# Performance work log

Measured on AMD Instinct MI355X. Metric: run time of the kernel, lower is better.

The kernel has to match this reference:

```python
import jax, jax.numpy as jnp
import numpy as np

N, D = 2048, 1024
H, KV, HD = 16, 4, 64
REPEATS = H // KV
SCALE = HD ** -0.5


def setup_inputs() -> dict:
    key = jax.random.key(0)
    ks = jax.random.split(key, 6)
    x = jax.random.normal(ks[0], (N, D), dtype=jnp.float32)
    # rotary tables: cos/sin of interleaved-pair angles (llama-style view_as_complex)
    pos = jnp.arange(N, dtype=jnp.float32)[:, None]
    inv_freq = 1.0 / (10000.0 ** (jnp.arange(0, HD, 2, dtype=jnp.float32) / HD))
    ang = pos * inv_freq[None, :]  # (N, HD//2)
    freqs_cos = jnp.cos(ang)
    freqs_sin = jnp.sin(ang)
    s = 0.02
    Wq = jax.random.normal(ks[1], (D, H * HD), dtype=jnp.float32) * s
    Wk = jax.random.normal(ks[2], (D, KV * HD), dtype=jnp.float32) * s
    Wv = jax.random.normal(ks[3], (D, KV * HD), dtype=jnp.float32) * s
    Wo = jax.random.normal(ks[4], (H * HD, D), dtype=jnp.float32) * s
    return {"x": x, "freqs_cos": freqs_cos, "freqs_sin": freqs_sin,
            "Wq": Wq, "Wk": Wk, "Wv": Wv, "Wo": Wo}


def _rope(t, cos, sin):
    # t: (N, heads, HD); interleaved complex pairs (even=real, odd=imag)
    tr = t[..., 0::2]
    ti = t[..., 1::2]
    c = cos[:, None, :]
    s = sin[:, None, :]
    out_r = tr * c - ti * s
    out_i = tr * s + ti * c
    return jnp.stack([out_r, out_i], axis=-1).reshape(t.shape)


def reference(x, freqs_cos, freqs_sin, Wq, Wk, Wv, Wo):
    n = x.shape[0]
    xq = (x @ Wq).reshape(n, H, HD)
    xk = (x @ Wk).reshape(n, KV, HD)
    xv = (x @ Wv).reshape(n, KV, HD)
    xq = _rope(xq, freqs_cos, freqs_sin)
    xk = _rope(xk, freqs_cos, freqs_sin)
    # repeat_kv along head dim (GQA)
    k = jnp.repeat(xk, REPEATS, axis=1)  # (n, H, HD)
    v = jnp.repeat(xv, REPEATS, axis=1)
    # memory_efficient_attention with mask=None: full attention over token axis
    scores = jnp.einsum('nhd,mhd->hnm', xq, k) * SCALE
    attn = jax.nn.softmax(scores, axis=-1)
    out = jnp.einsum('hnm,mhd->nhd', attn, v)
    return out.reshape(n, H * HD) @ Wo
```

## Files before the change

kernel.cpp:

```cpp
#include <hip/hip_runtime.h>

#define N_TOK 2048
#define DMODEL 1024
#define NH 16
#define NKV 4
#define HDIM 64
#define SCALE_LOG2E 0.1803368801111204f

typedef __attribute__((ext_vector_type(8))) short short8;
typedef __attribute__((ext_vector_type(4))) float f32x4;
typedef __attribute__((ext_vector_type(16))) float f32x16;
typedef __attribute__((ext_vector_type(2))) int i32x2;
typedef __attribute__((ext_vector_type(4))) unsigned int u32x4;
typedef unsigned short u16;
typedef unsigned int u32;

__device__ __forceinline__ u16 f2bf(float x) {
    u32 u = __float_as_uint(x);
    u += 0x7FFF + ((u >> 16) & 1);
    return (u16)(u >> 16);
}
__device__ __forceinline__ u32 pack2(float a, float b) {
    return (u32)f2bf(a) | ((u32)f2bf(b) << 16);
}
__device__ __forceinline__ u32 pack2t(float a, float b) {
    return __builtin_amdgcn_perm(__float_as_uint(b), __float_as_uint(a), 0x07060302u);
}

__device__ __forceinline__ void gload16(const u16* g, u16* l) {
    __builtin_amdgcn_global_load_lds(
        (const __attribute__((address_space(1))) unsigned int*)g,
        (__attribute__((address_space(3))) unsigned int*)l, 16, 0, 0);
}

__global__ __launch_bounds__(256) void prep(
    const float* __restrict__ Wq, const float* __restrict__ Wk,
    const float* __restrict__ Wv, const float* __restrict__ Wo,
    const float* __restrict__ x,
    u16* __restrict__ Wqt, u16* __restrict__ Wkt, u16* __restrict__ Wvt,
    u16* __restrict__ Wot, u16* __restrict__ xb)
{
    const int z = blockIdx.z;
    const int t = threadIdx.x;
    if (z == 4) {
        size_t base = ((size_t)(blockIdx.y * 16 + blockIdx.x)) * 8192;
#pragma unroll
        for (int i = 0; i < 8; ++i) {
            float4 v = *(const float4*)(x + base + i * 1024 + t * 4);
            uint2 p; p.x = pack2(v.x, v.y); p.y = pack2(v.z, v.w);
            *(uint2*)(xb + base + i * 1024 + t * 4) = p;
        }
        return;
    }
    const float* W; u16* Wt; int NC;
    if      (z == 0) { W = Wq; Wt = Wqt; NC = 1024; }
    else if (z == 1) { W = Wk; Wt = Wkt; NC = 256; }
    else if (z == 2) { W = Wv; Wt = Wvt; NC = 256; }
    else             { W = Wo; Wt = Wot; NC = 1024; }
    const int n0 = blockIdx.x * 64;
    if (n0 >= NC) return;
    const int k0 = blockIdx.y * 64;
    __shared__ float T[64][68];
    const int row = t >> 2, cs = (t & 3) * 16;
#pragma unroll
    for (int i = 0; i < 4; ++i)
        *(float4*)&T[row][cs + i * 4] =
            *(const float4*)(W + (size_t)(k0 + row) * NC + n0 + cs + i * 4);
    __syncthreads();
    const int nl = t >> 2, ks = (t & 3) * 16;
    u32 pk[8];
#pragma unroll
    for (int i = 0; i < 8; ++i)
        pk[i] = pack2(T[ks + 2 * i][nl], T[ks + 2 * i + 1][nl]);
    u16* dst = Wt + (size_t)(n0 + nl) * DMODEL + k0 + ks;
    uint4 w0; w0.x = pk[0]; w0.y = pk[1]; w0.z = pk[2]; w0.w = pk[3];
    uint4 w1; w1.x = pk[4]; w1.y = pk[5]; w1.z = pk[6]; w1.w = pk[7];
    *(uint4*)(dst) = w0;
    *(uint4*)(dst + 8) = w1;
}

__global__ __launch_bounds__(256, 3) void gemm_qkv(
    const u16* __restrict__ A,
    const u16* __restrict__ B0, const u16* __restrict__ B1, const u16* __restrict__ B2,
    u16* __restrict__ D0, u16* __restrict__ D1, u16* __restrict__ FVout,
    const float* __restrict__ fc, const float* __restrict__ fs)
{
    __shared__ u16 As[3][64][64];
    __shared__ u16 Bs[3][64][64];
    const int t = threadIdx.x;
    const int m0 = blockIdx.x * 64;
    const int by = blockIdx.y;

    const u16* Bt; int nl0, ep;
    u16* dbf = nullptr; int dstride = 0; float epsc = 1.f;
    if (by < 16)      { Bt = B0; nl0 = by * 64;        dbf = D0; ep = 1; dstride = 1024;
                        epsc = SCALE_LOG2E; }
    else if (by < 20) { Bt = B1; nl0 = (by - 16) * 64; dbf = D1; ep = 1; dstride = 256; }
    else              { Bt = B2; nl0 = (by - 20) * 64; ep = 2; }

    const int w = t >> 6, lane = t & 63;
    const int quad = lane >> 4, l15 = lane & 15;
    const int wm = (w >> 1) * 32, wn = (w & 1) * 32;
    const int rx = l15 & 7;

    const int sro = w * 16 + (lane >> 3);
    const int sco = ((lane & 7) ^ (lane >> 3)) * 8;
    const u16* ApL = A + (size_t)(m0 + sro) * DMODEL + sco;
    const u16* BpL = Bt + (size_t)(nl0 + sro) * DMODEL + sco;

    f32x4 acc[2][2];
#pragma unroll
    for (int i = 0; i < 2; ++i)
#pragma unroll
        for (int j = 0; j < 2; ++j) acc[i][j] = {0.f, 0.f, 0.f, 0.f};

#pragma unroll
    for (int k = 0; k < 2; ++k) {
        gload16(ApL + k * 8 * DMODEL, &As[0][w * 16 + k * 8][0]);
        gload16(BpL + k * 8 * DMODEL, &Bs[0][w * 16 + k * 8][0]);
    }
#pragma unroll
    for (int k = 0; k < 2; ++k) {
        gload16(ApL + k * 8 * DMODEL + 64, &As[1][w * 16 + k * 8][0]);
        gload16(BpL + k * 8 * DMODEL + 64, &Bs[1][w * 16 + k * 8][0]);
    }
    asm volatile("s_waitcnt vmcnt(4)" ::: "memory");
    __builtin_amdgcn_sched_barrier(0);
    __builtin_amdgcn_s_barrier();

    int cb = 0, nb = 1, pb = 2;
    for (int it = 0; it < 16; ++it) {
        if (it + 2 < 16) {
            const int kk = (it + 2) * 64;
#pragma unroll
            for (int k = 0; k < 2; ++k) {
                gload16(ApL + k * 8 * DMODEL + kk, &As[pb][w * 16 + k * 8][0]);
                gload16(BpL + k * 8 * DMODEL + kk, &Bs[pb][w * 16 + k * 8][0]);
            }
        }
#pragma unroll
        for (int c = 0; c < 2; ++c) {
            short8 af[2], bf[2];
#pragma unroll
            for (int i = 0; i < 2; ++i)
                af[i] = *(const short8*)&As[cb][wm + i * 16 + l15][((4 * c + quad) ^ rx) * 8];
#pragma unroll
            for (int j = 0; j < 2; ++j)
                bf[j] = *(const short8*)&Bs[cb][wn + j * 16 + l15][((4 * c + quad) ^ rx) * 8];
#pragma unroll
            for (int i = 0; i < 2; ++i)
#pragma unroll
                for (int j = 0; j < 2; ++j)
                    acc[i][j] = __builtin_amdgcn_mfma_f32_16x16x32_bf16(af[i], bf[j], acc[i][j], 0, 0, 0);
        }
        if (it + 2 < 16) asm volatile("s_waitcnt vmcnt(4)" ::: "memory");
        else             asm volatile("s_waitcnt vmcnt(0)" ::: "memory");
        __builtin_amdgcn_sched_barrier(0);
        __builtin_amdgcn_s_barrier();
        const int tmp = cb; cb = nb; nb = pb; pb = tmp;
    }

#pragma unroll
    for (int i = 0; i < 2; ++i)
#pragma unroll
        for (int j = 0; j < 2; ++j) {
            const int cl = nl0 + wn + j * 16 + l15;
            if (ep == 1) {
#pragma unroll
                for (int r4 = 0; r4 < 4; ++r4) {
                    const int r = m0 + wm + i * 16 + quad * 4 + r4;
                    float own = acc[i][j][r4];
                    float other = __shfl_xor(own, 1, 64);
                    const int p = (cl & 63) >> 1;
                    const float c = fc[r * 32 + p] * epsc, s = fs[r * 32 + p] * epsc;
                    float outv = ((cl & 1) == 0) ? (own * c - other * s)
                                                 : (other * s + own * c);
                    dbf[(size_t)r * dstride + cl] = f2bf(outv);
                }
            } else {
                const int rb = m0 + wm + i * 16 + quad * 4;
                const int g = cl >> 6, d = cl & 63;
                const int d2 = d >> 5, dl = d & 31;
                const int keyblk = rb >> 7, kg = (rb >> 5) & 3;
                const int kst = (rb >> 4) & 1, hb = (rb >> 3) & 1, jv = rb & 7;
                size_t idx = ((((((size_t)(g * 16 + keyblk) * 4 + kg) * 2 + kst) * 2 + d2)
                               * 2 + hb) * 32 + dl) * 8 + jv;
                uint2 pk;
                pk.x = pack2(acc[i][j][0], acc[i][j][1]);
                pk.y = pack2(acc[i][j][2], acc[i][j][3]);
                *(uint2*)(FVout + idx) = pk;
            }
        }
}

__global__ __launch_bounds__(256, 2) void gemm_out(
    const u16* __restrict__ A, const u16* __restrict__ Bt, float* __restrict__ Dout)
{
    __shared__ u16 As[3][64][64];
    __shared__ u16 Bs[3][64][64];
    const int t = threadIdx.x;
    const int m0 = blockIdx.x * 64;
    const int nl0 = blockIdx.y * 64;

    const int w = t >> 6, lane = t & 63;
    const int quad = lane >> 4, l15 = lane & 15;
    const int wm = (w >> 1) * 32, wn = (w & 1) * 32;
    const int rx = l15 & 7;

    const int sro = w * 16 + (lane >> 3);
    const int sco = ((lane & 7) ^ (lane >> 3)) * 8;
    const u16* ApL = A + (size_t)(m0 + sro) * DMODEL + sco;
    const u16* BpL = Bt + (size_t)(nl0 + sro) * DMODEL + sco;

    f32x4 acc[2][2];
#pragma unroll
    for (int i = 0; i < 2; ++i)
#pragma unroll
        for (int j = 0; j < 2; ++j) acc[i][j] = {0.f, 0.f, 0.f, 0.f};

#pragma unroll
    for (int k = 0; k < 2; ++k) {
        gload16(ApL + k * 8 * DMODEL, &As[0][w * 16 + k * 8][0]);
        gload16(BpL + k * 8 * DMODEL, &Bs[0][w * 16 + k * 8][0]);
    }
#pragma unroll
    for (int k = 0; k < 2; ++k) {
        gload16(ApL + k * 8 * DMODEL + 64, &As[1][w * 16 + k * 8][0]);
        gload16(BpL + k * 8 * DMODEL + 64, &Bs[1][w * 16 + k * 8][0]);
    }
    asm volatile("s_waitcnt vmcnt(4)" ::: "memory");
    __builtin_amdgcn_sched_barrier(0);
    __builtin_amdgcn_s_barrier();

    int cb = 0, nb = 1, pb = 2;
    for (int it = 0; it < 16; ++it) {
        if (it + 2 < 16) {
            const int kk = (it + 2) * 64;
#pragma unroll
            for (int k = 0; k < 2; ++k) {
                gload16(ApL + k * 8 * DMODEL + kk, &As[pb][w * 16 + k * 8][0]);
                gload16(BpL + k * 8 * DMODEL + kk, &Bs[pb][w * 16 + k * 8][0]);
            }
        }
#pragma unroll
        for (int c = 0; c < 2; ++c) {
            short8 af[2], bf[2];
#pragma unroll
            for (int i = 0; i < 2; ++i)
                af[i] = *(const short8*)&As[cb][wm + i * 16 + l15][((4 * c + quad) ^ rx) * 8];
#pragma unroll
            for (int j = 0; j < 2; ++j)
                bf[j] = *(const short8*)&Bs[cb][wn + j * 16 + l15][((4 * c + quad) ^ rx) * 8];
#pragma unroll
            for (int i = 0; i < 2; ++i)
#pragma unroll
                for (int j = 0; j < 2; ++j)
                    acc[i][j] = __builtin_amdgcn_mfma_f32_16x16x32_bf16(af[i], bf[j], acc[i][j], 0, 0, 0);
        }
        if (it + 2 < 16) asm volatile("s_waitcnt vmcnt(4)" ::: "memory");
        else             asm volatile("s_waitcnt vmcnt(0)" ::: "memory");
        __builtin_amdgcn_sched_barrier(0);
        __builtin_amdgcn_s_barrier();
        const int tmp = cb; cb = nb; nb = pb; pb = tmp;
    }

#pragma unroll
    for (int i = 0; i < 2; ++i)
#pragma unroll
        for (int j = 0; j < 2; ++j) {
            const int cl = nl0 + wn + j * 16 + l15;
#pragma unroll
            for (int r4 = 0; r4 < 4; ++r4) {
                const int r = m0 + wm + i * 16 + quad * 4 + r4;
                Dout[(size_t)r * 1024 + cl] = acc[i][j][r4];
            }
        }
}

__global__ __launch_bounds__(256, 2) void attn(
    const u16* __restrict__ Qb, const u16* __restrict__ Kb,
    const u16* __restrict__ FV, u16* __restrict__ Ob)
{
    __shared__ u16 Ks[2][2][64][72];

    const int t = threadIdx.x;
    const int n0 = blockIdx.x * 64;
    const int h = blockIdx.y, kvh = h >> 2;
    const int w = t >> 6, lane = t & 63;
    const int hi = lane >> 5, l31 = lane & 31;
    const int qgrp = w & 1, khalf = w >> 1;
    const int srow = t >> 1, ssel = (t & 1) * 32;
    const int khalf_s = srow >> 6, klocal = srow & 63;

    const short8 ones = {(short)0x3F80, (short)0x3F80, (short)0x3F80, (short)0x3F80,
                         (short)0x3F80, (short)0x3F80, (short)0x3F80, (short)0x3F80};

    const u16* qp = Qb + (size_t)(n0 + qgrp * 32 + l31) * (NH * HDIM) + h * HDIM + hi * 8;
    short8 qf[4];
#pragma unroll
    for (int s = 0; s < 4; ++s) qf[s] = *(const short8*)(qp + s * 16);

    const u16* kbase = Kb + (size_t)(khalf_s * 1024 + klocal) * (NKV * HDIM) + kvh * HDIM + ssel;
    const u16* fvb = FV + ((size_t)kvh * 16 * 8192) + (size_t)lane * 8;

    f32x16 o[2], o_l;
#pragma unroll
    for (int d2 = 0; d2 < 2; ++d2)
#pragma unroll
        for (int r = 0; r < 16; ++r) o[d2][r] = 0.f;
#pragma unroll
    for (int r = 0; r < 16; ++r) o_l[r] = 0.f;

#pragma unroll
    for (int c = 0; c < 4; ++c)
        *(uint4*)&Ks[0][khalf_s][klocal][ssel + c * 8] = *(const uint4*)(kbase + c * 8);
    __syncthreads();

    for (int rd = 0; rd < 16; ++rd) {
        const int cur = rd & 1, nxt = cur ^ 1;
        const int rdn = (rd + 1) & 15;
        uint4 kr[4];
#pragma unroll
        for (int c = 0; c < 4; ++c)
            kr[c] = *(const uint4*)(kbase + (size_t)(rdn * 64) * (NKV * HDIM) + c * 8);

        short8 vf[2][2][2];
#pragma unroll
        for (int kg = 0; kg < 2; ++kg) {
            const int kg_global = khalf * 32 + rd * 2 + kg;
            const int keyblk = kg_global >> 2, kgi = kg_global & 3;
#pragma unroll
            for (int s = 0; s < 2; ++s)
#pragma unroll
                for (int d2 = 0; d2 < 2; ++d2)
                    vf[kg][s][d2] = *(const short8*)(fvb +
                        ((((size_t)keyblk * 4 + kgi) * 2 + s) * 2 + d2) * 512);
        }

#pragma unroll
        for (int kg = 0; kg < 2; ++kg) {
            f32x16 sa;
#pragma unroll
            for (int r = 0; r < 16; ++r) sa[r] = 0.f;
            __builtin_amdgcn_s_setprio(1);
#pragma unroll
            for (int s = 0; s < 4; ++s) {
                short8 kf = *(const short8*)&Ks[cur][khalf][kg * 32 + l31][s * 16 + hi * 8];
                sa = __builtin_amdgcn_mfma_f32_32x32x16_bf16(kf, qf[s], sa, 0, 0, 0);
            }
            __builtin_amdgcn_s_setprio(0);
            float p[16];
#pragma unroll
            for (int r = 0; r < 16; ++r) p[r] = __builtin_amdgcn_exp2f(sa[r]);
            const u32 A0 = pack2t(p[0],  p[1]);
            const u32 B0 = pack2t(p[2],  p[3]);
            const u32 C0 = pack2t(p[4],  p[5]);
            const u32 D0 = pack2t(p[6],  p[7]);
            const u32 E0 = pack2t(p[8],  p[9]);
            const u32 F0 = pack2t(p[10], p[11]);
            const u32 G0 = pack2t(p[12], p[13]);
            const u32 H0 = pack2t(p[14], p[15]);
            i32x2 X = __builtin_amdgcn_permlane32_swap((int)A0, (int)C0, false, false);
            i32x2 Y = __builtin_amdgcn_permlane32_swap((int)B0, (int)D0, false, false);
            i32x2 Z = __builtin_amdgcn_permlane32_swap((int)E0, (int)G0, false, false);
            i32x2 U = __builtin_amdgcn_permlane32_swap((int)F0, (int)H0, false, false);
            u32x4 t0 = {(u32)X.x, (u32)Y.x, (u32)X.y, (u32)Y.y};
            u32x4 t1 = {(u32)Z.x, (u32)U.x, (u32)Z.y, (u32)U.y};
            const short8 ap0 = __builtin_bit_cast(short8, t0);
            const short8 ap1 = __builtin_bit_cast(short8, t1);
            __builtin_amdgcn_s_setprio(1);
#pragma unroll
            for (int d2 = 0; d2 < 2; ++d2) {
                o[d2] = __builtin_amdgcn_mfma_f32_32x32x16_bf16(ap0, vf[kg][0][d2], o[d2], 0, 0, 0);
                o[d2] = __builtin_amdgcn_mfma_f32_32x32x16_bf16(ap1, vf[kg][1][d2], o[d2], 0, 0, 0);
            }
            o_l = __builtin_amdgcn_mfma_f32_32x32x16_bf16(ap0, ones, o_l, 0, 0, 0);
            o_l = __builtin_amdgcn_mfma_f32_32x32x16_bf16(ap1, ones, o_l, 0, 0, 0);
            __builtin_amdgcn_s_setprio(0);
        }
#pragma unroll
        for (int c = 0; c < 4; ++c)
            *(uint4*)&Ks[nxt][khalf_s][klocal][ssel + c * 8] = kr[c];
        __syncthreads();
    }

    float* Xf = (float*)&Ks[0][0][0][0];
    if (khalf == 1) {
#pragma unroll
        for (int d2 = 0; d2 < 2; ++d2)
#pragma unroll
            for (int r = 0; r < 16; ++r) {
                const int q32 = (r & 3) + 8 * (r >> 2) + 4 * hi;
                Xf[qgrp * 2048 + q32 * 64 + d2 * 32 + l31] = o[d2][r];
            }
        if (l31 == 0) {
#pragma unroll
            for (int r = 0; r < 16; ++r) {
                const int q32 = (r & 3) + 8 * (r >> 2) + 4 * hi;
                Xf[4096 + qgrp * 32 + q32] = o_l[r];
            }
        }
    }
    __syncthreads();
    if (khalf == 0) {
        float linv[16];
#pragma unroll
        for (int r = 0; r < 16; ++r) {
            const int q32 = (r & 3) + 8 * (r >> 2) + 4 * hi;
            linv[r] = 1.f / (o_l[r] + Xf[4096 + qgrp * 32 + q32]);
        }
#pragma unroll
        for (int d2 = 0; d2 < 2; ++d2)
#pragma unroll
            for (int r = 0; r < 16; ++r) {
                const int q32 = (r & 3) + 8 * (r >> 2) + 4 * hi;
                const float val = o[d2][r] + Xf[qgrp * 2048 + q32 * 64 + d2 * 32 + l31];
                const int qrow = n0 + qgrp * 32 + q32;
                Ob[(size_t)qrow * (NH * HDIM) + h * HDIM + d2 * 32 + l31] = f2bf(val * linv[r]);
            }
    }
}

extern "C" void kernel_launch(void* const* d_in, const int* in_sizes, int n_in,
                              void* d_out, int out_size, void* d_ws, size_t ws_size,
                              hipStream_t stream) {
    const float* x  = (const float*)d_in[0];
    const float* fc = (const float*)d_in[1];
    const float* fs = (const float*)d_in[2];
    const float* Wq = (const float*)d_in[3];
    const float* Wk = (const float*)d_in[4];
    const float* Wv = (const float*)d_in[5];
    const float* Wo = (const float*)d_in[6];
    float* out = (float*)d_out;

    u16* ws  = (u16*)d_ws;
    u16* xb  = ws;
    u16* Wqt = xb  + (size_t)2048 * 1024;
    u16* Wkt = Wqt + (size_t)1024 * 1024;
    u16* Wvt = Wkt + (size_t)256 * 1024;
    u16* Wot = Wvt + (size_t)256 * 1024;
    u16* qb  = Wot + (size_t)1024 * 1024;
    u16* kb  = qb  + (size_t)2048 * 1024;
    u16* fv  = kb  + (size_t)2048 * 256;
    u16* aob = fv  + (size_t)256 * 2048;

    prep<<<dim3(16, 16, 5), dim3(256), 0, stream>>>(Wq, Wk, Wv, Wo, x,
                                                    Wqt, Wkt, Wvt, Wot, xb);
    gemm_qkv<<<dim3(32, 24), dim3(256), 0, stream>>>(xb, Wqt, Wkt, Wvt,
                                                     qb, kb, fv, fc, fs);
    attn<<<dim3(32, 16), dim3(256), 0, stream>>>(qb, kb, fv, aob);
    gemm_out<<<dim3(32, 16), dim3(256), 0, stream>>>(aob, Wot, out);
}
```

Baseline: 128.7 us.

## Store K in MFMA fragment layout and load directly from global, dropping LDS staging

```diff
diff --git a/kernel.cpp b/kernel.cpp
--- a/kernel.cpp
+++ b/kernel.cpp
@@ -82,7 +82,7 @@
 __global__ __launch_bounds__(256, 3) void gemm_qkv(
     const u16* __restrict__ A,
     const u16* __restrict__ B0, const u16* __restrict__ B1, const u16* __restrict__ B2,
-    u16* __restrict__ D0, u16* __restrict__ D1, u16* __restrict__ FVout,
+    u16* __restrict__ D0, u16* __restrict__ FKout, u16* __restrict__ FVout,
     const float* __restrict__ fc, const float* __restrict__ fs)
 {
     __shared__ u16 As[3][64][64];
@@ -92,10 +92,9 @@
     const int by = blockIdx.y;
 
     const u16* Bt; int nl0, ep;
-    u16* dbf = nullptr; int dstride = 0; float epsc = 1.f;
-    if (by < 16)      { Bt = B0; nl0 = by * 64;        dbf = D0; ep = 1; dstride = 1024;
-                        epsc = SCALE_LOG2E; }
-    else if (by < 20) { Bt = B1; nl0 = (by - 16) * 64; dbf = D1; ep = 1; dstride = 256; }
+    float epsc = 1.f;
+    if (by < 16)      { Bt = B0; nl0 = by * 64;        ep = 1; epsc = SCALE_LOG2E; }
+    else if (by < 20) { Bt = B1; nl0 = (by - 16) * 64; ep = 3; }
     else              { Bt = B2; nl0 = (by - 20) * 64; ep = 2; }
 
     const int w = t >> 6, lane = t & 63;
@@ -175,7 +174,25 @@
                     const float c = fc[r * 32 + p] * epsc, s = fs[r * 32 + p] * epsc;
                     float outv = ((cl & 1) == 0) ? (own * c - other * s)
                                                  : (other * s + own * c);
-                    dbf[(size_t)r * dstride + cl] = f2bf(outv);
+                    D0[(size_t)r * 1024 + cl] = f2bf(outv);
+                }
+            } else if (ep == 3) {
+#pragma unroll
+                for (int r4 = 0; r4 < 4; ++r4) {
+                    const int r = m0 + wm + i * 16 + quad * 4 + r4;
+                    float own = acc[i][j][r4];
+                    float other = __shfl_xor(own, 1, 64);
+                    const int p = (cl & 63) >> 1;
+                    const float c = fc[r * 32 + p], s = fs[r * 32 + p];
+                    float outv = ((cl & 1) == 0) ? (own * c - other * s)
+                                                 : (other * s + own * c);
+                    const int kvh2 = cl >> 6, d = cl & 63;
+                    const int s2 = d >> 4, hi2 = (d >> 3) & 1, jv = d & 7;
+                    const int kh2 = r >> 10, rd2 = (r >> 6) & 15;
+                    const int kg2 = (r >> 5) & 1, l31v = r & 31;
+                    size_t idx = ((((((size_t)(kvh2 * 2 + kh2) * 16 + rd2) * 2 + kg2)
+                                    * 4 + s2) * 2 + hi2) * 32 + l31v) * 8 + jv;
+                    FKout[idx] = f2bf(outv);
                 }
             } else {
                 const int rb = m0 + wm + i * 16 + quad * 4;
@@ -278,10 +295,10 @@
 }
 
 __global__ __launch_bounds__(256, 2) void attn(
-    const u16* __restrict__ Qb, const u16* __restrict__ Kb,
+    const u16* __restrict__ Qb, const u16* __restrict__ FK,
     const u16* __restrict__ FV, u16* __restrict__ Ob)
 {
-    __shared__ u16 Ks[2][2][64][72];
+    __shared__ float Xf[4160];
 
     const int t = threadIdx.x;
     const int n0 = blockIdx.x * 64;
@@ -289,8 +306,6 @@
     const int w = t >> 6, lane = t & 63;
     const int hi = lane >> 5, l31 = lane & 31;
     const int qgrp = w & 1, khalf = w >> 1;
-    const int srow = t >> 1, ssel = (t & 1) * 32;
-    const int khalf_s = srow >> 6, klocal = srow & 63;
 
     const short8 ones = {(short)0x3F80, (short)0x3F80, (short)0x3F80, (short)0x3F80,
                          (short)0x3F80, (short)0x3F80, (short)0x3F80, (short)0x3F80};
@@ -300,8 +315,8 @@
 #pragma unroll
     for (int s = 0; s < 4; ++s) qf[s] = *(const short8*)(qp + s * 16);
 
-    const u16* kbase = Kb + (size_t)(khalf_s * 1024 + klocal) * (NKV * HDIM) + kvh * HDIM + ssel;
-    const u16* fvb = FV + ((size_t)kvh * 16 * 8192) + (size_t)lane * 8;
+    const u16* fkb = FK + ((size_t)(kvh * 2 + khalf)) * 65536 + (size_t)lane * 8;
+    const u16* fvb = FV + ((size_t)kvh) * 131072 + (size_t)lane * 8;
 
     f32x16 o[2], o_l;
 #pragma unroll
@@ -311,18 +326,14 @@
 #pragma unroll
     for (int r = 0; r < 16; ++r) o_l[r] = 0.f;
 
-#pragma unroll
-    for (int c = 0; c < 4; ++c)
-        *(uint4*)&Ks[0][khalf_s][klocal][ssel + c * 8] = *(const uint4*)(kbase + c * 8);
-    __syncthreads();
+    short8 kfa[4], kfb2[4];
+#pragma unroll
+    for (int s = 0; s < 4; ++s) kfa[s]  = *(const short8*)(fkb + s * 512);
+#pragma unroll
+    for (int s = 0; s < 4; ++s) kfb2[s] = *(const short8*)(fkb + 2048 + s * 512);
 
     for (int rd = 0; rd < 16; ++rd) {
-        const int cur = rd & 1, nxt = cur ^ 1;
         const int rdn = (rd + 1) & 15;
-        uint4 kr[4];
-#pragma unroll
-        for (int c = 0; c < 4; ++c)
-            kr[c] = *(const uint4*)(kbase + (size_t)(rdn * 64) * (NKV * HDIM) + c * 8);
 
         short8 vf[2][2][2];
 #pragma unroll
@@ -337,29 +348,25 @@
                         ((((size_t)keyblk * 4 + kgi) * 2 + s) * 2 + d2) * 512);
         }
 
-#pragma unroll
-        for (int kg = 0; kg < 2; ++kg) {
-            f32x16 sa;
-#pragma unroll
-            for (int r = 0; r < 16; ++r) sa[r] = 0.f;
-            __builtin_amdgcn_s_setprio(1);
-#pragma unroll
-            for (int s = 0; s < 4; ++s) {
-                short8 kf = *(const short8*)&Ks[cur][khalf][kg * 32 + l31][s * 16 + hi * 8];
-                sa = __builtin_amdgcn_mfma_f32_32x32x16_bf16(kf, qf[s], sa, 0, 0, 0);
-            }
-            __builtin_amdgcn_s_setprio(0);
+        f32x16 sa;
+#pragma unroll
+        for (int r = 0; r < 16; ++r) sa[r] = 0.f;
+        __builtin_amdgcn_s_setprio(1);
+#pragma unroll
+        for (int s = 0; s < 4; ++s)
+            sa = __builtin_amdgcn_mfma_f32_32x32x16_bf16(kfa[s], qf[s], sa, 0, 0, 0);
+        __builtin_amdgcn_s_setprio(0);
+#pragma unroll
+        for (int s = 0; s < 4; ++s)
+            kfa[s] = *(const short8*)(fkb + (size_t)rdn * 4096 + s * 512);
+        {
             float p[16];
 #pragma unroll
             for (int r = 0; r < 16; ++r) p[r] = __builtin_amdgcn_exp2f(sa[r]);
-            const u32 A0 = pack2t(p[0],  p[1]);
-            const u32 B0 = pack2t(p[2],  p[3]);
-            const u32 C0 = pack2t(p[4],  p[5]);
-            const u32 D0 = pack2t(p[6],  p[7]);
-            const u32 E0 = pack2t(p[8],  p[9]);
-            const u32 F0 = pack2t(p[10], p[11]);
-            const u32 G0 = pack2t(p[12], p[13]);
-            const u32 H0 = pack2t(p[14], p[15]);
+            const u32 A0 = pack2t(p[0],  p[1]),  B0 = pack2t(p[2],  p[3]);
+            const u32 C0 = pack2t(p[4],  p[5]),  D0 = pack2t(p[6],  p[7]);
+            const u32 E0 = pack2t(p[8],  p[9]),  F0 = pack2t(p[10], p[11]);
+            const u32 G0 = pack2t(p[12], p[13]), H0 = pack2t(p[14], p[15]);
             i32x2 X = __builtin_amdgcn_permlane32_swap((int)A0, (int)C0, false, false);
             i32x2 Y = __builtin_amdgcn_permlane32_swap((int)B0, (int)D0, false, false);
             i32x2 Z = __builtin_amdgcn_permlane32_swap((int)E0, (int)G0, false, false);
@@ -371,20 +378,52 @@
             __builtin_amdgcn_s_setprio(1);
 #pragma unroll
             for (int d2 = 0; d2 < 2; ++d2) {
-                o[d2] = __builtin_amdgcn_mfma_f32_32x32x16_bf16(ap0, vf[kg][0][d2], o[d2], 0, 0, 0);
-                o[d2] = __builtin_amdgcn_mfma_f32_32x32x16_bf16(ap1, vf[kg][1][d2], o[d2], 0, 0, 0);
+                o[d2] = __builtin_amdgcn_mfma_f32_32x32x16_bf16(ap0, vf[0][0][d2], o[d2], 0, 0, 0);
+                o[d2] = __builtin_amdgcn_mfma_f32_32x32x16_bf16(ap1, vf[0][1][d2], o[d2], 0, 0, 0);
             }
             o_l = __builtin_amdgcn_mfma_f32_32x32x16_bf16(ap0, ones, o_l, 0, 0, 0);
             o_l = __builtin_amdgcn_mfma_f32_32x32x16_bf16(ap1, ones, o_l, 0, 0, 0);
             __builtin_amdgcn_s_setprio(0);
         }
-#pragma unroll
-        for (int c = 0; c < 4; ++c)
-            *(uint4*)&Ks[nxt][khalf_s][klocal][ssel + c * 8] = kr[c];
-        __syncthreads();
-    }
-
-    float* Xf = (float*)&Ks[0][0][0][0];
+
+#pragma unroll
+        for (int r = 0; r < 16; ++r) sa[r] = 0.f;
+        __builtin_amdgcn_s_setprio(1);
+#pragma unroll
+        for (int s = 0; s < 4; ++s)
+            sa = __builtin_amdgcn_mfma_f32_32x32x16_bf16(kfb2[s], qf[s], sa, 0, 0, 0);
+        __builtin_amdgcn_s_setprio(0);
+#pragma unroll
+        for (int s = 0; s < 4; ++s)
+            kfb2[s] = *(const short8*)(fkb + (size_t)rdn * 4096 + 2048 + s * 512);
+        {
+            float p[16];
+#pragma unroll
+            for (int r = 0; r < 16; ++r) p[r] = __builtin_amdgcn_exp2f(sa[r]);
+            const u32 A0 = pack2t(p[0],  p[1]),  B0 = pack2t(p[2],  p[3]);
+            const u32 C0 = pack2t(p[4],  p[5]),  D0 = pack2t(p[6],  p[7]);
+            const u32 E0 = pack2t(p[8],  p[9]),  F0 = pack2t(p[10], p[11]);
+            const u32 G0 = pack2t(p[12], p[13]), H0 = pack2t(p[14], p[15]);
+            i32x2 X = __builtin_amdgcn_permlane32_swap((int)A0, (int)C0, false, false);
+            i32x2 Y = __builtin_amdgcn_permlane32_swap((int)B0, (int)D0, false, false);
+            i32x2 Z = __builtin_amdgcn_permlane32_swap((int)E0, (int)G0, false, false);
+            i32x2 U = __builtin_amdgcn_permlane32_swap((int)F0, (int)H0, false, false);
+            u32x4 t0 = {(u32)X.x, (u32)Y.x, (u32)X.y, (u32)Y.y};
+            u32x4 t1 = {(u32)Z.x, (u32)U.x, (u32)Z.y, (u32)U.y};
+            const short8 ap0 = __builtin_bit_cast(short8, t0);
+            const short8 ap1 = __builtin_bit_cast(short8, t1);
+            __builtin_amdgcn_s_setprio(1);
+#pragma unroll
+            for (int d2 = 0; d2 < 2; ++d2) {
+                o[d2] = __builtin_amdgcn_mfma_f32_32x32x16_bf16(ap0, vf[1][0][d2], o[d2], 0, 0, 0);
+                o[d2] = __builtin_amdgcn_mfma_f32_32x32x16_bf16(ap1, vf[1][1][d2], o[d2], 0, 0, 0);
+            }
+            o_l = __builtin_amdgcn_mfma_f32_32x32x16_bf16(ap0, ones, o_l, 0, 0, 0);
+            o_l = __builtin_amdgcn_mfma_f32_32x32x16_bf16(ap1, ones, o_l, 0, 0, 0);
+            __builtin_amdgcn_s_setprio(0);
+        }
+    }
+
     if (khalf == 1) {
 #pragma unroll
         for (int d2 = 0; d2 < 2; ++d2)
@@ -440,14 +479,14 @@
     u16* Wvt = Wkt + (size_t)256 * 1024;
     u16* Wot = Wvt + (size_t)256 * 1024;
     u16* qb  = Wot + (size_t)1024 * 1024;
-    u16* kb  = qb  + (size_t)2048 * 1024;
-    u16* fv  = kb  + (size_t)2048 * 256;
+    u16* fk  = qb  + (size_t)2048 * 1024;
+    u16* fv  = fk  + (size_t)2048 * 256;
     u16* aob = fv  + (size_t)256 * 2048;
 
     prep<<<dim3(16, 16, 5), dim3(256), 0, stream>>>(Wq, Wk, Wv, Wo, x,
                                                     Wqt, Wkt, Wvt, Wot, xb);
     gemm_qkv<<<dim3(32, 24), dim3(256), 0, stream>>>(xb, Wqt, Wkt, Wvt,
-                                                     qb, kb, fv, fc, fs);
-    attn<<<dim3(32, 16), dim3(256), 0, stream>>>(qb, kb, fv, aob);
+                                                     qb, fk, fv, fc, fs);
+    attn<<<dim3(32, 16), dim3(256), 0, stream>>>(qb, fk, fv, aob);
     gemm_out<<<dim3(32, 16), dim3(256), 0, stream>>>(aob, Wot, out);
 }
```

Result: no change. 126.4 us (median of 2 runs) (-1.8%).
